# Optimization experiments

Measured on AMD Instinct MI355X. Metric: run time of the kernel, lower is better.

The kernel has to match this reference:

```python
import jax, jax.numpy as jnp
import numpy as np

HEAD_NUM = 16
EMBED_DIM = 512


def setup_inputs() -> dict:
    key = jax.random.key(0)
    k1, k2, k3, k4, k5 = jax.random.split(key, 5)
    B, N, D = 8, 2048, EMBED_DIM
    x = jax.random.normal(k1, (B, N, D), dtype=jnp.float32)
    dis_matrix = jax.random.uniform(k2, (B, N, N), dtype=jnp.float32)
    s = 1.0 / np.sqrt(D)
    Wq = jax.random.normal(k3, (D, D), dtype=jnp.float32) * s
    Wk = jax.random.normal(k4, (D, D), dtype=jnp.float32) * s
    Wv = jax.random.normal(k5, (D, D), dtype=jnp.float32) * s
    alpha = jnp.float32(1.0)
    return {"x": x, "dis_matrix": dis_matrix, "Wq": Wq, "Wk": Wk, "Wv": Wv, "alpha": alpha}


def _split_heads(t, H):
    # [B, N, D] -> [B, H, N, D//H]
    B, N, D = t.shape
    return t.reshape(B, N, H, D // H).transpose(0, 2, 1, 3)


def reference(x, dis_matrix, Wq, Wk, Wv, alpha):
    B, N, D = x.shape
    H = HEAD_NUM
    # nn.Linear(bias=False): y = x @ W.T
    q = _split_heads(x @ Wq.T, H)  # [B,H,N,dk]
    k = _split_heads(x @ Wk.T, H)
    v = _split_heads(x @ Wv.T, H)
    log2n = jnp.float32(np.log2(N))
    dis_weight = jnp.exp(-alpha * log2n * dis_matrix)  # [B,N,N]
    k_weight = jnp.exp(k)
    # contract over source node i -> target node j
    weight_1 = jnp.einsum('bij,bhik->bhjk', dis_weight, k_weight * v)
    weight_2 = jnp.einsum('bij,bhik->bhjk', dis_weight, k_weight)
    out = jax.nn.sigmoid(q) * (weight_1 / weight_2)  # [B,H,N,dk]
    return out.transpose(0, 2, 1, 3).reshape(B, N, D)
```

## Files before the change

kernel.cpp:

```cpp
#include <hip/hip_runtime.h>
#include <math.h>
#include <stdint.h>


typedef __bf16 bf16_t;
typedef __attribute__((ext_vector_type(4))) __bf16 bf16x4;
typedef __attribute__((ext_vector_type(8))) __bf16 bf16x8;
typedef __attribute__((ext_vector_type(4))) float f32x4;

#define MFMA_BF16(a, b, c) __builtin_amdgcn_mfma_f32_16x16x32_bf16((a), (b), (c), 0, 0, 0)

static __device__ __forceinline__ void async_ld16(const bf16_t* g, bf16_t* lds) {
  __builtin_amdgcn_global_load_lds(
      reinterpret_cast<__attribute__((address_space(1))) unsigned int*>(
          reinterpret_cast<uintptr_t>(g)),
      reinterpret_cast<__attribute__((address_space(3))) unsigned int*>(
          reinterpret_cast<uintptr_t>(lds)),
      16, 0, 0);
}

static __device__ __forceinline__ f32x4 async_ldg_f32x4(const float* p) {
  f32x4 r;
  asm volatile("global_load_dwordx4 %0, %1, off" : "=&v"(r) : "v"(p) : "memory");
  return r;
}

#define WAITV(N)                                          \
  do {                                                    \
    asm volatile("s_waitcnt vmcnt(" #N ")" ::: "memory"); \
    __builtin_amdgcn_sched_barrier(0);                    \
  } while (0)

template <int ROWS>
static __device__ __forceinline__ void stage3(const bf16_t* g, int ldg, bf16_t* lds,
                                              int wv, int lane) {
  const int r_in = lane >> 3;
  const int cpos = lane & 7;
#pragma unroll
  for (int s = 0; s < ROWS / 32; ++s) {
    int rbase = wv * (ROWS / 4) + s * 8;
    int row = rbase + r_in;
    int cg = cpos ^ (row & 7);
    async_ld16(g + (size_t)row * ldg + cg * 8, lds + rbase * 64 + lane * 8);
  }
}

static __device__ __forceinline__ bf16x8 frag3(const bf16_t* lds, int row16,
                                               int l15, int quad, int kc) {
  int p = (quad | (kc << 2)) ^ (l15 & 7);
  return *(const bf16x8*)&lds[(row16 + l15) * 64 + p * 8];
}

__global__ __launch_bounds__(256) void cvt_all(const float* __restrict__ x,
                                               const float* __restrict__ wq,
                                               const float* __restrict__ wk,
                                               const float* __restrict__ wv,
                                               bf16_t* __restrict__ xb,
                                               bf16_t* __restrict__ wall) {
  int i = blockIdx.x * 256 + threadIdx.x;
  if (i >= 2293760) return;
  const float* src;
  bf16_t* dst;
  int off;
  if (i < 2097152) {
    src = x; dst = xb; off = i;
  } else {
    int j = i - 2097152;
    int sel = j >> 16;
    off = j & 65535;
    src = (sel == 0) ? wq : (sel == 1) ? wk : wv;
    dst = wall + (size_t)sel * 262144;
  }
  f32x4 f = ((const f32x4*)src)[off];
  bf16x4 o;
  o[0] = (bf16_t)f[0]; o[1] = (bf16_t)f[1]; o[2] = (bf16_t)f[2]; o[3] = (bf16_t)f[3];
  ((bf16x4*)dst)[off] = o;
}

__global__ __launch_bounds__(256, 4) void proj_dw(const bf16_t* __restrict__ A,
                                                  const bf16_t* __restrict__ W,
                                                  bf16_t* __restrict__ qs,
                                                  bf16_t* __restrict__ kwT,
                                                  bf16_t* __restrict__ kwvT) {
  __shared__ __align__(16) char pool[32768];
  const int tid = threadIdx.x;
  const int sub = blockIdx.x;
  const int m_blk = sub / 12, n_blk = sub % 12;
  bf16_t* As = (bf16_t*)pool;
  const int K = 512;
  const int wv = tid >> 6, lane = tid & 63;
  const int l15 = lane & 15, quad = lane >> 4;
  const int wm = wv >> 1, wn = wv & 1;
  const bf16_t* Am = A + (size_t)(m_blk * 128) * K;
  const int b = m_blk >> 4;

  if (n_blk < 4) {
    bf16_t* Bsq = (bf16_t*)(pool + 16384);
    const int c_loc = n_blk * 128;
    f32x4 acc[4][4];
#pragma unroll
    for (int a = 0; a < 4; ++a)
#pragma unroll
      for (int c = 0; c < 4; ++c) acc[a][c] = (f32x4){0.f, 0.f, 0.f, 0.f};

    for (int k0 = 0; k0 < K; k0 += 64) {
      stage3<128>(Am + k0, K, As, wv, lane);
      stage3<128>(W + (size_t)c_loc * K + k0, K, Bsq, wv, lane);
      __syncthreads();
#pragma unroll
      for (int kc = 0; kc < 2; ++kc) {
        bf16x8 a[4], bb[4];
#pragma unroll
        for (int mf = 0; mf < 4; ++mf) a[mf] = frag3(As, wm * 64 + mf * 16, l15, quad, kc);
#pragma unroll
        for (int nf = 0; nf < 4; ++nf) bb[nf] = frag3(Bsq, wn * 64 + nf * 16, l15, quad, kc);
#pragma unroll
        for (int mf = 0; mf < 4; ++mf)
#pragma unroll
          for (int nf = 0; nf < 4; ++nf) acc[mf][nf] = MFMA_BF16(a[mf], bb[nf], acc[mf][nf]);
      }
      __syncthreads();
    }
#pragma unroll
    for (int mf = 0; mf < 4; ++mf)
#pragma unroll
      for (int nf = 0; nf < 4; ++nf) {
        int j16 = (m_blk & 15) * 8 + wm * 4 + mf;
        int c16 = n_blk * 8 + wn * 4 + nf;
        bf16x4 o;
#pragma unroll
        for (int r = 0; r < 4; ++r)
          o[r] = (bf16_t)(1.0f / (1.0f + __expf(-acc[mf][nf][r])));
        size_t off = (((size_t)b * 128 + j16) * 32 + c16) * 256 + quad * 64 + l15 * 4;
        *(bf16x4*)&qs[off] = o;
      }
  } else {
    bf16_t* Bk = (bf16_t*)(pool + 16384);
    bf16_t* Bv = (bf16_t*)(pool + 24576);
    const int c_loc = (n_blk - 4) * 64;
    f32x4 acck[4][2], accv[4][2];
#pragma unroll
    for (int a = 0; a < 4; ++a)
#pragma unroll
      for (int c = 0; c < 2; ++c) {
        acck[a][c] = (f32x4){0.f, 0.f, 0.f, 0.f};
        accv[a][c] = (f32x4){0.f, 0.f, 0.f, 0.f};
      }
    const bf16_t* Wk = W + (size_t)(512 + c_loc) * K;
    const bf16_t* Wv = W + (size_t)(1024 + c_loc) * K;

    for (int k0 = 0; k0 < K; k0 += 64) {
      stage3<128>(Am + k0, K, As, wv, lane);
      stage3<64>(Wk + k0, K, Bk, wv, lane);
      stage3<64>(Wv + k0, K, Bv, wv, lane);
      __syncthreads();
#pragma unroll
      for (int kc = 0; kc < 2; ++kc) {
        bf16x8 a[4], bk[2], bv[2];
#pragma unroll
        for (int mf = 0; mf < 4; ++mf) a[mf] = frag3(As, wm * 64 + mf * 16, l15, quad, kc);
#pragma unroll
        for (int nf = 0; nf < 2; ++nf) {
          bk[nf] = frag3(Bk, wn * 32 + nf * 16, l15, quad, kc);
          bv[nf] = frag3(Bv, wn * 32 + nf * 16, l15, quad, kc);
        }
#pragma unroll
        for (int mf = 0; mf < 4; ++mf)
#pragma unroll
          for (int nf = 0; nf < 2; ++nf) {
            acck[mf][nf] = MFMA_BF16(a[mf], bk[nf], acck[mf][nf]);
            accv[mf][nf] = MFMA_BF16(a[mf], bv[nf], accv[mf][nf]);
          }
      }
      __syncthreads();
    }

    bf16_t* Lk = (bf16_t*)pool;
    bf16_t* Lv = (bf16_t*)(pool + 8704);
    const int t0 = (m_blk * 128) & 2047;
#pragma unroll
    for (int ci = 0; ci < 2; ++ci) {
      if (wn == ci) {
#pragma unroll
        for (int mf = 0; mf < 4; ++mf)
#pragma unroll
          for (int nf = 0; nf < 2; ++nf) {
            int cl = nf * 16 + l15;
            int tl = wm * 64 + mf * 16 + quad * 4;
#pragma unroll
            for (int r = 0; r < 4; ++r) {
              float kw = __expf(acck[mf][nf][r]);
              Lk[cl * 136 + tl + r] = (bf16_t)kw;
              Lv[cl * 136 + tl + r] = (bf16_t)(kw * accv[mf][nf][r]);
            }
          }
      }
      __syncthreads();
      {
        int rowt = tid >> 3, colt = (tid & 7) * 16;
        int c = c_loc + ci * 32 + rowt;
        size_t g = ((size_t)b * 512 + c) * 2048 + t0 + colt;
        *(bf16x8*)&kwT[g] = *(const bf16x8*)&Lk[rowt * 136 + colt];
        *(bf16x8*)&kwT[g + 8] = *(const bf16x8*)&Lk[rowt * 136 + colt + 8];
        *(bf16x8*)&kwvT[g] = *(const bf16x8*)&Lv[rowt * 136 + colt];
        *(bf16x8*)&kwvT[g + 8] = *(const bf16x8*)&Lv[rowt * 136 + colt + 8];
      }
      __syncthreads();
    }
  }
}

__global__ __launch_bounds__(512, 2) void main_gemm(const float* __restrict__ dis,
                                                    const bf16_t* __restrict__ kwvT,
                                                    const bf16_t* __restrict__ kwT,
                                                    const bf16_t* __restrict__ qs,
                                                    const float* __restrict__ alpha,
                                                    float* __restrict__ out) {
  extern __shared__ __align__(16) char smem_raw[];
  bf16_t* const lds = (bf16_t*)smem_raw;
  const int K = 2048;
  const int tid = threadIdx.x;
  const int wv = tid >> 6, lane = tid & 63;
  const int l15 = lane & 15, quad = lane >> 4;
  const int bi = blockIdx.x;
  const int b = bi & 7, nbb = (bi >> 3) & 3, mb = bi >> 5;
  const int wm = wv >> 2, wn = wv & 3;
  const int r_in = lane >> 3, cpos = lane & 7;
  const int cg = cpos ^ r_in;

  const float coef = -alpha[0] * 11.0f;

  const bf16_t* const BvB = kwvT + (size_t)b * 512 * K;
  const bf16_t* const BkB = kwT + (size_t)b * 512 * K;

  const int jb = tid >> 3, ib = tid & 7;
  const float* const disB = dis + (size_t)b * 2048 * 2048 + (size_t)(mb * 256 + jb * 4);

  const bf16_t* bSrc[4];
  int bDst[4];
#pragma unroll
  for (int cb = 0; cb < 4; ++cb) {
    const int base1 = (cb & 1) * 128 + (cb >> 1) * 32;
    const int rowbase = base1 + (wv >> 2) * 64 + (wv & 3) * 8;
    const int row = rowbase + r_in;
    const int type = (row >> 4) & 1;
    const int crow = nbb * 128 + (row >> 5) * 16 + (row & 15);
    bSrc[cb] = (type ? BkB : BvB) + (size_t)crow * K + cg * 8;
    bDst[cb] = 16384 + rowbase * 64 + lane * 8;
  }

  f32x4 acc[8][4];
#pragma unroll
  for (int m = 0; m < 8; ++m)
#pragma unroll
    for (int n = 0; n < 4; ++n) acc[m][n] = (f32x4){0.f, 0.f, 0.f, 0.f};

  bf16x8 a[8];
  bf16x8 b0[4];
  bf16x8 b1[4];
  f32x4 rA0[4], rA1[4];

#define STAGE_B(dst, cb, koff) async_ld16(bSrc[cb] + (koff), lds + (dst)*32768 + bDst[cb])

#define CONVW(dstbuf, h, rr)                                                     \
  do {                                                                           \
    bf16_t* An_ = lds + (dstbuf)*32768;                                          \
    const int il_ = (h)*32 + ib * 4;                                             \
    _Pragma("unroll") for (int cc_ = 0; cc_ < 4; ++cc_) {                        \
      const int jl_ = jb * 4 + cc_;                                              \
      bf16x4 w_;                                                                 \
      w_[0] = (bf16_t)__expf(coef * (rr)[0][cc_]);                               \
      w_[1] = (bf16_t)__expf(coef * (rr)[1][cc_]);                               \
      w_[2] = (bf16_t)__expf(coef * (rr)[2][cc_]);                               \
      w_[3] = (bf16_t)__expf(coef * (rr)[3][cc_]);                               \
      *(bf16x4*)&An_[jl_ * 64 + (((il_ >> 3) ^ (jl_ & 7)) << 3) + (il_ & 4)] = w_; \
    }                                                                            \
  } while (0)

#define LOADA(As_, mh)                                                             \
  do {                                                                             \
    _Pragma("unroll") for (int mf = 0; mf < 4; ++mf)                               \
        _Pragma("unroll") for (int kc = 0; kc < 2; ++kc)                           \
            a[mf * 2 + kc] =                                                       \
        frag3((As_), wm * 128 + (mh)*64 + mf * 16, l15, quad, kc);                 \
  } while (0)

#define LOADB(Bs_, dstarr, nh)                                                     \
  do {                                                                             \
    _Pragma("unroll") for (int nf = 0; nf < 2; ++nf)                               \
        _Pragma("unroll") for (int kc = 0; kc < 2; ++kc)                           \
            dstarr[nf * 2 + kc] =                                                  \
        frag3((Bs_), wn * 64 + (nh)*32 + nf * 16, l15, quad, kc);                  \
  } while (0)

#define MFMA_PH(mh, nh, barr)                                                      \
  do {                                                                             \
    __builtin_amdgcn_s_setprio(1);                                                 \
    _Pragma("unroll") for (int kc = 0; kc < 2; ++kc)                               \
        _Pragma("unroll") for (int mf = 0; mf < 4; ++mf)                           \
            _Pragma("unroll") for (int nf = 0; nf < 2; ++nf)                       \
                acc[(mh)*4 + mf][(nh)*2 + nf] =                                    \
        MFMA_BF16(a[mf * 2 + kc], barr[nf * 2 + kc], acc[(mh)*4 + mf][(nh)*2 + nf]); \
    __builtin_amdgcn_s_setprio(0);                                                 \
  } while (0)

  STAGE_B(0, 0, 0); STAGE_B(0, 1, 0); STAGE_B(0, 2, 0); STAGE_B(0, 3, 0);
#pragma unroll
  for (int r = 0; r < 4; ++r) rA0[r] = async_ldg_f32x4(disB + (size_t)(ib * 4 + r) * 2048);
#pragma unroll
  for (int r = 0; r < 4; ++r) rA1[r] = async_ldg_f32x4(disB + (size_t)(32 + ib * 4 + r) * 2048);
  WAITV(0);
  CONVW(0, 0, rA0);
  CONVW(0, 1, rA1);
  __syncthreads();

  for (int t = 0; t < 32; ++t) {
    const int c = t & 1;
    const int nx = c ^ 1;
    const bf16_t* As_c = lds + c * 32768;
    const bf16_t* Bs_c = As_c + 16384;
    if (t < 31) {
      const int ko = (t + 1) * 64;
      STAGE_B(nx, 0, ko); STAGE_B(nx, 1, ko); STAGE_B(nx, 2, ko); STAGE_B(nx, 3, ko);
      const float* dp = disB + (size_t)(t + 1) * 64 * 2048;
#pragma unroll
      for (int r = 0; r < 4; ++r) rA0[r] = async_ldg_f32x4(dp + (size_t)(ib * 4 + r) * 2048);
#pragma unroll
      for (int r = 0; r < 4; ++r) rA1[r] = async_ldg_f32x4(dp + (size_t)(32 + ib * 4 + r) * 2048);
    }
    LOADA(As_c, 0);
    LOADB(Bs_c, b0, 0);
    __builtin_amdgcn_s_barrier();
    MFMA_PH(0, 0, b0);
    __builtin_amdgcn_s_barrier();
    LOADB(Bs_c, b1, 1);
    __builtin_amdgcn_s_barrier();
    MFMA_PH(0, 1, b1);
    __builtin_amdgcn_s_barrier();
    if (t < 31) { WAITV(4); CONVW(nx, 0, rA0); }
    LOADA(As_c, 1);
    __builtin_amdgcn_s_barrier();
    MFMA_PH(1, 1, b1);
    __builtin_amdgcn_s_barrier();
    if (t < 31) { WAITV(0); CONVW(nx, 1, rA1); }
    MFMA_PH(1, 0, b0);
    __syncthreads();
  }

#undef STAGE_B
#undef CONVW
#undef LOADA
#undef LOADB
#undef MFMA_PH

#pragma unroll
  for (int mf = 0; mf < 8; ++mf)
#pragma unroll
    for (int p = 0; p < 2; ++p) {
      f32x4 w1 = acc[mf][2 * p];
      f32x4 w2 = acc[mf][2 * p + 1];
      const int j16 = mb * 16 + wm * 8 + mf;
      const int c16 = nbb * 8 + wn * 2 + p;
      size_t qoff = (((size_t)b * 128 + j16) * 32 + c16) * 256 + quad * 64 + l15 * 4;
      bf16x4 qv = *(const bf16x4*)&qs[qoff];
      const int ccol = c16 * 16 + l15;
#pragma unroll
      for (int r = 0; r < 4; ++r) {
        const int j = j16 * 16 + quad * 4 + r;
        out[((size_t)b * 2048 + j) * 512 + ccol] = (float)qv[r] * (w1[r] / w2[r]);
      }
    }
}

extern "C" void kernel_launch(void* const* d_in, const int* in_sizes, int n_in,
                              void* d_out, int out_size, void* d_ws, size_t ws_size,
                              hipStream_t stream) {
  const float* x = (const float*)d_in[0];
  const float* dis = (const float*)d_in[1];
  const float* Wq = (const float*)d_in[2];
  const float* Wk = (const float*)d_in[3];
  const float* Wv = (const float*)d_in[4];
  const float* alpha = (const float*)d_in[5];
  float* out = (float*)d_out;

  char* p = (char*)d_ws;
  bf16_t* x_bf = (bf16_t*)p;  p += (size_t)16384 * 512 * 2;
  bf16_t* Wall = (bf16_t*)p;  p += (size_t)1536 * 512 * 2;
  bf16_t* kwT  = (bf16_t*)p;  p += (size_t)8 * 512 * 2048 * 2;
  bf16_t* kwvT = (bf16_t*)p;  p += (size_t)8 * 512 * 2048 * 2;
  bf16_t* qs_bf = (bf16_t*)p; p += (size_t)16384 * 512 * 2;
  if ((size_t)(p - (char*)d_ws) > ws_size) return;

  static bool attr_done = false;
  if (!attr_done) {
    hipFuncSetAttribute(reinterpret_cast<const void*>(main_gemm),
                        hipFuncAttributeMaxDynamicSharedMemorySize, 131072);
    attr_done = true;
  }

  cvt_all<<<8960, 256, 0, stream>>>(x, Wq, Wk, Wv, x_bf, Wall);
  proj_dw<<<1536, 256, 0, stream>>>(x_bf, Wall, qs_bf, kwT, kwvT);
  main_gemm<<<256, 512, 131072, stream>>>(dis, kwvT, kwT, qs_bf, alpha, out);
}
```

Before: 379.4 us.

## Issue dis loads first and use fine-grained vmcnt waits with peeled tail

The distance-matrix loads for the next tile are now issued before the B-tile async LDS stages. Each CONVW waits only on the loads it actually needs, through partial vmcnt counts placed before the barriers. Full __syncthreads calls become explicit lgkm/vm waits plus s_barrier, and the last iteration is peeled to remove the t<31 branches. The goal is to overlap the next tile's global traffic with MFMA work and shorten barrier stalls. The WAITV(2) before each iteration boundary may let some B-stage loads still be in flight when the next iteration reads LDS, which risks a race.

```diff
diff --git a/kernel.cpp b/kernel.cpp
--- a/kernel.cpp
+++ b/kernel.cpp
@@ -29,6 +29,12 @@
   do {                                                    \
     asm volatile("s_waitcnt vmcnt(" #N ")" ::: "memory"); \
     __builtin_amdgcn_sched_barrier(0);                    \
+  } while (0)
+
+#define WAIT_LGKM0()                                        \
+  do {                                                      \
+    asm volatile("s_waitcnt lgkmcnt(0)" ::: "memory");      \
+    __builtin_amdgcn_sched_barrier(0);                      \
   } while (0)
 
 template <int ROWS>
@@ -262,6 +268,15 @@
 
 #define STAGE_B(dst, cb, koff) async_ld16(bSrc[cb] + (koff), lds + (dst)*32768 + bDst[cb])
 
+#define ISSUE_DIS(tt)                                                              \
+  do {                                                                             \
+    const float* dp_ = disB + (size_t)(tt)*64 * 2048;                              \
+    _Pragma("unroll") for (int r = 0; r < 4; ++r)                                  \
+        rA0[r] = async_ldg_f32x4(dp_ + (size_t)(ib * 4 + r) * 2048);               \
+    _Pragma("unroll") for (int r = 0; r < 4; ++r)                                  \
+        rA1[r] = async_ldg_f32x4(dp_ + (size_t)(32 + ib * 4 + r) * 2048);          \
+  } while (0)
+
 #define CONVW(dstbuf, h, rr)                                                     \
   do {                                                                           \
     bf16_t* An_ = lds + (dstbuf)*32768;                                          \
@@ -304,50 +319,69 @@
     __builtin_amdgcn_s_setprio(0);                                                 \
   } while (0)
 
+  ISSUE_DIS(0);
   STAGE_B(0, 0, 0); STAGE_B(0, 1, 0); STAGE_B(0, 2, 0); STAGE_B(0, 3, 0);
-#pragma unroll
-  for (int r = 0; r < 4; ++r) rA0[r] = async_ldg_f32x4(disB + (size_t)(ib * 4 + r) * 2048);
-#pragma unroll
-  for (int r = 0; r < 4; ++r) rA1[r] = async_ldg_f32x4(disB + (size_t)(32 + ib * 4 + r) * 2048);
-  WAITV(0);
+  WAITV(4);
   CONVW(0, 0, rA0);
   CONVW(0, 1, rA1);
-  __syncthreads();
-
-  for (int t = 0; t < 32; ++t) {
+  WAITV(2);
+  WAIT_LGKM0();
+  __builtin_amdgcn_s_barrier();
+
+  for (int t = 0; t < 31; ++t) {
     const int c = t & 1;
     const int nx = c ^ 1;
     const bf16_t* As_c = lds + c * 32768;
     const bf16_t* Bs_c = As_c + 16384;
-    if (t < 31) {
-      const int ko = (t + 1) * 64;
-      STAGE_B(nx, 0, ko); STAGE_B(nx, 1, ko); STAGE_B(nx, 2, ko); STAGE_B(nx, 3, ko);
-      const float* dp = disB + (size_t)(t + 1) * 64 * 2048;
-#pragma unroll
-      for (int r = 0; r < 4; ++r) rA0[r] = async_ldg_f32x4(dp + (size_t)(ib * 4 + r) * 2048);
-#pragma unroll
-      for (int r = 0; r < 4; ++r) rA1[r] = async_ldg_f32x4(dp + (size_t)(32 + ib * 4 + r) * 2048);
-    }
+    const int ko = (t + 1) * 64;
+    ISSUE_DIS(t + 1);
+    STAGE_B(nx, 0, ko); STAGE_B(nx, 1, ko); STAGE_B(nx, 2, ko); STAGE_B(nx, 3, ko);
     LOADA(As_c, 0);
     LOADB(Bs_c, b0, 0);
     __builtin_amdgcn_s_barrier();
     MFMA_PH(0, 0, b0);
+    WAITV(12);
     __builtin_amdgcn_s_barrier();
     LOADB(Bs_c, b1, 1);
     __builtin_amdgcn_s_barrier();
     MFMA_PH(0, 1, b1);
-    __builtin_amdgcn_s_barrier();
-    if (t < 31) { WAITV(4); CONVW(nx, 0, rA0); }
+    WAITV(8);
+    __builtin_amdgcn_s_barrier();
+    CONVW(nx, 0, rA0);
     LOADA(As_c, 1);
     __builtin_amdgcn_s_barrier();
     MFMA_PH(1, 1, b1);
-    __builtin_amdgcn_s_barrier();
-    if (t < 31) { WAITV(0); CONVW(nx, 1, rA1); }
+    WAITV(4);
+    __builtin_amdgcn_s_barrier();
+    CONVW(nx, 1, rA1);
     MFMA_PH(1, 0, b0);
-    __syncthreads();
+    WAITV(2);
+    WAIT_LGKM0();
+    __builtin_amdgcn_s_barrier();
+  }
+
+  {
+    const bf16_t* As_c = lds + 32768;
+    const bf16_t* Bs_c = As_c + 16384;
+    LOADA(As_c, 0);
+    LOADB(Bs_c, b0, 0);
+    __builtin_amdgcn_s_barrier();
+    MFMA_PH(0, 0, b0);
+    WAITV(0);
+    __builtin_amdgcn_s_barrier();
+    LOADB(Bs_c, b1, 1);
+    __builtin_amdgcn_s_barrier();
+    MFMA_PH(0, 1, b1);
+    __builtin_amdgcn_s_barrier();
+    LOADA(As_c, 1);
+    __builtin_amdgcn_s_barrier();
+    MFMA_PH(1, 1, b1);
+    __builtin_amdgcn_s_barrier();
+    MFMA_PH(1, 0, b0);
   }
 
 #undef STAGE_B
+#undef ISSUE_DIS
 #undef CONVW
 #undef LOADA
 #undef LOADB
```

Measured after the change: 379.1 us. Within noise of the previous version (-0.1%).
